# Performance work log

Hardware: AMD Instinct MI355X
Metric: run time of the kernel (lower is better)

Reference implementation:

```python
import jax, jax.numpy as jnp
import numpy as np

B, N, DIM, H, D, S = 4, 16384, 256, 8, 64, 64
INNER = H * D


def setup_inputs() -> dict:
    key = jax.random.key(0)
    ks = jax.random.split(key, 10)
    f = lambda k, shp, s: jax.random.normal(k, shp, jnp.float32) * s
    return {
        "x": jax.random.normal(ks[0], (B, N, DIM), jnp.float32),
        "Wx": f(ks[1], (INNER, DIM), 0.02), "bx": jnp.zeros((INNER,), jnp.float32),
        "Wfx": f(ks[2], (INNER, DIM), 0.02), "bfx": jnp.zeros((INNER,), jnp.float32),
        "Wslice": f(ks[3], (S, D), 0.125), "bslice": jnp.zeros((S,), jnp.float32),
        "temperature": jnp.full((1, H, 1, 1), 0.5, jnp.float32),
        "Wq": f(ks[4], (D, D), 0.125),
        "Wk": f(ks[5], (D, D), 0.125),
        "Wv": f(ks[6], (D, D), 0.125),
        "attn_scale": jnp.full((1, H, 1, 1), 10.0, jnp.float32),
        "slice_res_scale": jnp.full((1,), 0.1, jnp.float32),
        "Wout": f(ks[7], (DIM, INNER), 0.02), "bout": jnp.zeros((DIM,), jnp.float32),
    }


def reference(x, Wx, bx, Wfx, bfx, Wslice, bslice, temperature,
              Wq, Wk, Wv, attn_scale, slice_res_scale, Wout, bout):
    b, n, _ = x.shape
    # project and split heads -> [b, h, n, d]
    fx = (x @ Wfx.T + bfx).reshape(b, n, H, D).transpose(0, 2, 1, 3)
    xm = (x @ Wx.T + bx).reshape(b, n, H, D).transpose(0, 2, 1, 3)
    temp = jnp.clip(temperature, 1e-4)
    slice_logits = (xm @ Wslice.T + bslice) / temp              # [b,h,n,S]
    w = jax.nn.softmax(slice_logits, axis=-1)                   # slice weights
    slice_norm = w.sum(axis=2)                                  # [b,h,S]
    tok = jnp.einsum('bhnc,bhng->bhgc', fx, w)                  # [b,h,S,d]
    tok = tok / (slice_norm + 1e-5)[:, :, :, None]
    # small cross-slice attention (cosine, shared kv across heads)
    q = tok @ Wq.T                                              # [b,h,S,d]
    kv = tok.mean(axis=1, keepdims=True)                        # [b,1,S,d]
    k = kv @ Wk.T
    v = kv @ Wv.T
    qn = q / jnp.maximum(jnp.linalg.norm(q, axis=-1, keepdims=True), 1e-12)
    kn = k / jnp.maximum(jnp.linalg.norm(k, axis=-1, keepdims=True), 1e-12)
    logits = jnp.einsum('bhgd,bzsd->bhgs', qn, kn) * attn_scale  # z==1 broadcast
    attn = jax.nn.softmax(logits, axis=-1)
    out_tok = jnp.einsum('bhgs,bzsd->bhgd', attn, v)
    out_tok = out_tok + slice_res_scale * tok
    # broadcast slice tokens back to points
    out_x = jnp.einsum('bhgc,bhng->bhnc', out_tok, w)           # [b,h,n,d]
    out_x = out_x.transpose(0, 2, 1, 3).reshape(b, n, H * D)
    return out_x @ Wout.T + bout
```

## Files before the change

### kernel.cpp

```cpp
#include <hip/hip_runtime.h>
#include <math.h>

#define BQ   4
#define NTOK 16384
#define DIMM 256
#define HH   8
#define DDIM 64
#define SSL  64
#define INNERD 512
#define BN_TOK (BQ*NTOK)

typedef __attribute__((ext_vector_type(8))) short short8;
typedef __attribute__((ext_vector_type(4))) float f32x4;

__device__ inline float bf2f(unsigned short u) {
    union { float f; unsigned int i; } v; v.i = ((unsigned int)u) << 16; return v.f;
}
__device__ inline unsigned short f2bf(float f) {
    union { float f; unsigned int i; } v; v.f = f;
    unsigned int r = v.i + 0x7FFFu + ((v.i >> 16) & 1u);
    return (unsigned short)(r >> 16);
}

__device__ __forceinline__ void gl_lds16(const void* g, void* l) {
    __builtin_amdgcn_global_load_lds(
        (const __attribute__((address_space(1))) unsigned int*)g,
        (__attribute__((address_space(3))) unsigned int*)l, 16, 0, 0);
}

__global__ void k_prep(const float* __restrict__ Wx, const float* __restrict__ bx,
                       const float* __restrict__ Wfx, const float* __restrict__ bfx,
                       const float* __restrict__ Wslice, const float* __restrict__ bslice,
                       unsigned short* __restrict__ Wcatb, float* __restrict__ bcat)
{
    int row = blockIdx.x;
    int t = threadIdx.x;
    if (row < 512) {
        for (int c = t; c < 256; c += 64) Wcatb[row*256 + c] = f2bf(Wfx[row*256 + c]);
        if (t == 0) bcat[row] = bfx[row];
    } else {
        int r = row - 512, h = r >> 6, s = r & 63;
        for (int c = t; c < 256; c += 64) {
            float acc = 0.f;
            for (int d = 0; d < 64; ++d)
                acc += Wslice[s*64 + d] * Wx[(h*64 + d)*256 + c];
            Wcatb[row*256 + c] = f2bf(acc);
        }
        if (t == 0) {
            float acc = bslice[s];
            for (int d = 0; d < 64; ++d) acc += Wslice[s*64 + d] * bx[h*64 + d];
            bcat[row] = acc;
        }
    }
}

__global__ void k_xcast(const float* __restrict__ x, unsigned short* __restrict__ xb)
{
    size_t i = ((size_t)blockIdx.x*256 + threadIdx.x)*8;
    float4 a = *(const float4*)(x + i);
    float4 b = *(const float4*)(x + i + 4);
    *(ushort4*)(xb + i)     = make_ushort4(f2bf(a.x), f2bf(a.y), f2bf(a.z), f2bf(a.w));
    *(ushort4*)(xb + i + 4) = make_ushort4(f2bf(b.x), f2bf(b.y), f2bf(b.z), f2bf(b.w));
}

__global__ __launch_bounds__(256) void k_gemm1(
    const unsigned short* __restrict__ Xb, const unsigned short* __restrict__ Wb,
    const float* __restrict__ bias, const float* __restrict__ temperature,
    unsigned short* __restrict__ fx_t, unsigned short* __restrict__ wbuf)
{
    __shared__ unsigned short As[128*32];
    __shared__ unsigned short Bs[128*32];
    int bid = blockIdx.x;
    int rt = bid >> 3, ct = bid & 7;
    int m0 = rt*128, n0 = ct*128;
    int tid = threadIdx.x;
    int lane = tid & 63, w = tid >> 6;
    int wr = w >> 1, wc = w & 1;
    int lr = lane & 15, lq = lane >> 4;

    f32x4 acc[4][4];
#pragma unroll
    for (int i = 0; i < 4; i++)
#pragma unroll
        for (int j = 0; j < 4; j++) acc[i][j] = (f32x4)(0.f);

    int r0 = tid >> 2, kq0 = (tid & 3) * 8;

    for (int k0 = 0; k0 < 256; k0 += 32) {
        __syncthreads();
        gl_lds16(Xb + (size_t)(m0 + r0)*256 + k0 + kq0,      &As[(size_t)tid*8]);
        gl_lds16(Xb + (size_t)(m0 + 64 + r0)*256 + k0 + kq0, &As[(size_t)(tid+256)*8]);
        gl_lds16(Wb + (size_t)(n0 + r0)*256 + k0 + kq0,      &Bs[(size_t)tid*8]);
        gl_lds16(Wb + (size_t)(n0 + 64 + r0)*256 + k0 + kq0, &Bs[(size_t)(tid+256)*8]);
        __syncthreads();
        short8 af[4], bf[4];
#pragma unroll
        for (int i = 0; i < 4; i++) {
            af[i] = *(const short8*)&As[(wr*64 + i*16 + lr)*32 + lq*8];
            bf[i] = *(const short8*)&Bs[(wc*64 + i*16 + lr)*32 + lq*8];
        }
#pragma unroll
        for (int i = 0; i < 4; i++)
#pragma unroll
            for (int j = 0; j < 4; j++)
                acc[i][j] = __builtin_amdgcn_mfma_f32_16x16x32_bf16(af[i], bf[j], acc[i][j], 0, 0, 0);
    }

    float bv[4];
#pragma unroll
    for (int j = 0; j < 4; j++) bv[j] = bias[n0 + wc*64 + j*16 + lr];

    if (n0 < 512) {
        int h = (n0 + wc*64) >> 6;
        int batch = m0 >> 14;
#pragma unroll
        for (int i = 0; i < 4; i++) {
            int tokbase = m0 + wr*64 + i*16 + lq*4;
            int nloc = tokbase & (NTOK-1);
#pragma unroll
            for (int j = 0; j < 4; j++) {
                int d = j*16 + lr;
                ushort4 pk = make_ushort4(
                    f2bf(acc[i][j][0] + bv[j]), f2bf(acc[i][j][1] + bv[j]),
                    f2bf(acc[i][j][2] + bv[j]), f2bf(acc[i][j][3] + bv[j]));
                *(ushort4*)(fx_t + ((size_t)(batch*8 + h)*64 + d)*NTOK + nloc) = pk;
            }
        }
    } else {
        int h = (n0 - 512 + wc*64) >> 6;
        float it = 1.f / fmaxf(temperature[h], 1e-4f);
        int colbase = (n0 - 512) + wc*64;
#pragma unroll
        for (int i = 0; i < 4; i++) {
            int tokbase = m0 + wr*64 + i*16 + lq*4;
#pragma unroll
            for (int r = 0; r < 4; r++) {
                float v[4];
#pragma unroll
                for (int j = 0; j < 4; j++) v[j] = (acc[i][j][r] + bv[j]) * it;
                float mx = fmaxf(fmaxf(v[0], v[1]), fmaxf(v[2], v[3]));
                mx = fmaxf(mx, __shfl_xor(mx, 1));
                mx = fmaxf(mx, __shfl_xor(mx, 2));
                mx = fmaxf(mx, __shfl_xor(mx, 4));
                mx = fmaxf(mx, __shfl_xor(mx, 8));
                float e[4], sm = 0.f;
#pragma unroll
                for (int j = 0; j < 4; j++) { e[j] = __expf(v[j] - mx); sm += e[j]; }
                sm += __shfl_xor(sm, 1);
                sm += __shfl_xor(sm, 2);
                sm += __shfl_xor(sm, 4);
                sm += __shfl_xor(sm, 8);
                float inv = 1.f / sm;
                size_t rowoff = (size_t)(tokbase + r)*512 + colbase + lr;
#pragma unroll
                for (int j = 0; j < 4; j++)
                    wbuf[rowoff + j*16] = f2bf(e[j] * inv);
            }
        }
    }
}

__global__ __launch_bounds__(256) void k_tok(
    const unsigned short* __restrict__ wbuf, const unsigned short* __restrict__ fx_t,
    float* __restrict__ tok_acc, float* __restrict__ norm_acc)
{
    __shared__ unsigned short As[64*32];
    __shared__ unsigned short Bs[64*32];
    __shared__ float nsm[256];
    int chunk = blockIdx.x;
    int bh = blockIdx.y;
    int b = bh >> 3, h = bh & 7;
    int n0 = chunk * 512;
    int tid = threadIdx.x;
    int lane = tid & 63, w = tid >> 6;
    int lr = lane & 15, lq = lane >> 4;

    f32x4 acc[4];
#pragma unroll
    for (int j = 0; j < 4; j++) acc[j] = (f32x4)(0.f);
    float nacc = 0.f;

    int sN = tid & 63, qN = tid >> 6;

    for (int kk = 0; kk < 512; kk += 32) {
        __syncthreads();
        gl_lds16(fx_t + ((size_t)bh*64 + (tid>>2))*NTOK + n0 + kk + (tid&3)*8,
                 &Bs[(size_t)tid*8]);
        {
            int tk = tid >> 3;
            int s8 = (tid & 7) * 8;
            short8 g = *(const short8*)(wbuf +
                ((size_t)(b*NTOK + n0 + kk + tk))*512 + h*64 + s8);
#pragma unroll
            for (int j = 0; j < 8; j++)
                As[(s8 + j)*32 + tk] = ((unsigned short*)&g)[j];
        }
        __syncthreads();
        {
            float ns = 0.f;
#pragma unroll
            for (int k = 0; k < 8; k++) ns += bf2f(As[sN*32 + qN*8 + k]);
            nacc += ns;
        }
        short8 af = *(const short8*)&As[(w*16 + lr)*32 + lq*8];
#pragma unroll
        for (int j = 0; j < 4; j++) {
            short8 bf = *(const short8*)&Bs[(j*16 + lr)*32 + lq*8];
            acc[j] = __builtin_amdgcn_mfma_f32_16x16x32_bf16(af, bf, acc[j], 0, 0, 0);
        }
    }

#pragma unroll
    for (int j = 0; j < 4; j++) {
        int d = j*16 + lr;
#pragma unroll
        for (int r = 0; r < 4; r++) {
            int s = w*16 + lq*4 + r;
            atomicAdd(&tok_acc[((size_t)bh*64 + s)*64 + d], acc[j][r]);
        }
    }
    __syncthreads();
    nsm[tid] = nacc;
    __syncthreads();
    if (tid < 64)
        atomicAdd(&norm_acc[bh*64 + tid],
                  nsm[tid] + nsm[tid+64] + nsm[tid+128] + nsm[tid+192]);
}

__global__ void k_fintok(float* __restrict__ tok, const float* __restrict__ norm)
{
    int bh = blockIdx.x, tid = threadIdx.x;
    for (int idx = tid; idx < 4096; idx += 256) {
        int s = idx >> 6;
        tok[(size_t)bh*4096 + idx] /= (norm[bh*64 + s] + 1e-5f);
    }
}

__global__ __launch_bounds__(256) void k_kv(
    const float* __restrict__ tok, const float* __restrict__ Wk, const float* __restrict__ Wv,
    float* __restrict__ kn_out, float* __restrict__ v_out)
{
    __shared__ float KV[64][65];
    __shared__ float TMP[64][65];
    __shared__ float rn[64];
    int b = blockIdx.x, tid = threadIdx.x;
    for (int idx = tid; idx < 4096; idx += 256) {
        float s = 0.f;
        for (int h = 0; h < 8; ++h) s += tok[((size_t)(b*8 + h))*4096 + idx];
        KV[idx >> 6][idx & 63] = s * 0.125f;
    }
    __syncthreads();
    for (int idx = tid; idx < 4096; idx += 256) {
        int s = idx >> 6, d = idx & 63;
        float a = 0.f;
        for (int e = 0; e < 64; ++e) a += KV[s][e] * Wk[d*64 + e];
        TMP[s][d] = a;
    }
    __syncthreads();
    if (tid < 64) {
        float a = 0.f;
        for (int d = 0; d < 64; ++d) { float x = TMP[tid][d]; a += x*x; }
        rn[tid] = fmaxf(sqrtf(a), 1e-12f);
    }
    __syncthreads();
    for (int idx = tid; idx < 4096; idx += 256) {
        int s = idx >> 6, d = idx & 63;
        kn_out[(size_t)b*4096 + idx] = TMP[s][d] / rn[s];
    }
    for (int idx = tid; idx < 4096; idx += 256) {
        int s = idx >> 6, d = idx & 63;
        float a = 0.f;
        for (int e = 0; e < 64; ++e) a += KV[s][e] * Wv[d*64 + e];
        v_out[(size_t)b*4096 + idx] = a;
    }
}

__global__ __launch_bounds__(256) void k_attn(
    const float* __restrict__ tok, const float* __restrict__ Wq,
    const float* __restrict__ kn, const float* __restrict__ vbuf,
    const float* __restrict__ attn_scale, const float* __restrict__ srs,
    float* __restrict__ out_tok)
{
    __shared__ float Q[64][65];
    __shared__ float KN[64][65];
    __shared__ float L[64][65];
    __shared__ float rn[64];
    int h = blockIdx.x & 7, b = blockIdx.x >> 3;
    int bh = b*8 + h;
    int tid = threadIdx.x;
    for (int idx = tid; idx < 4096; idx += 256)
        KN[idx >> 6][idx & 63] = kn[(size_t)b*4096 + idx];
    __syncthreads();
    for (int idx = tid; idx < 4096; idx += 256) {
        int g = idx >> 6, d = idx & 63;
        float a = 0.f;
        for (int e = 0; e < 64; ++e) a += tok[(size_t)bh*4096 + g*64 + e] * Wq[d*64 + e];
        Q[g][d] = a;
    }
    __syncthreads();
    if (tid < 64) {
        float a = 0.f;
        for (int d = 0; d < 64; ++d) { float x = Q[tid][d]; a += x*x; }
        rn[tid] = fmaxf(sqrtf(a), 1e-12f);
    }
    __syncthreads();
    float scale = attn_scale[h];
    for (int idx = tid; idx < 4096; idx += 256) {
        int g = idx >> 6, s = idx & 63;
        float a = 0.f;
        for (int e = 0; e < 64; ++e) a += Q[g][e] * KN[s][e];
        L[g][s] = a / rn[g] * scale;
    }
    __syncthreads();
    if (tid < 64) {
        float mx = -1e30f;
        for (int s = 0; s < 64; ++s) mx = fmaxf(mx, L[tid][s]);
        float sm = 0.f;
        for (int s = 0; s < 64; ++s) { float e = expf(L[tid][s]-mx); L[tid][s] = e; sm += e; }
        float inv = 1.f/sm;
        for (int s = 0; s < 64; ++s) L[tid][s] *= inv;
    }
    __syncthreads();
    float srsv = srs[0];
    for (int idx = tid; idx < 4096; idx += 256) {
        int g = idx >> 6, d = idx & 63;
        float a = 0.f;
        for (int s = 0; s < 64; ++s) a += L[g][s] * vbuf[(size_t)b*4096 + s*64 + d];
        out_tok[(size_t)bh*4096 + idx] = a + srsv * tok[(size_t)bh*4096 + idx];
    }
}

__global__ __launch_bounds__(256) void k_mt(
    const float* __restrict__ out_tok, const float* __restrict__ Wout,
    unsigned short* __restrict__ MTb)
{
    __shared__ float Wt[64][68];
    __shared__ float Ot[64][68];
    int jt = blockIdx.x, h = blockIdx.y, b = blockIdx.z;
    int j0 = jt * 64;
    int tid = threadIdx.x;
    int tx = tid & 15, ty = tid >> 4;
#pragma unroll
    for (int i = 0; i < 4; i++) {
        int flat = tid + i*256;
        int r = flat >> 4;
        int c4 = (flat & 15) * 4;
        float4 wv = *(const float4*)(Wout + (size_t)(j0+r)*512 + h*64 + c4);
        Wt[c4+0][r]=wv.x; Wt[c4+1][r]=wv.y; Wt[c4+2][r]=wv.z; Wt[c4+3][r]=wv.w;
        float4 ov = *(const float4*)(out_tok + ((size_t)(b*8+h)*64 + r)*64 + c4);
        Ot[c4+0][r]=ov.x; Ot[c4+1][r]=ov.y; Ot[c4+2][r]=ov.z; Ot[c4+3][r]=ov.w;
    }
    __syncthreads();
    float acc[4][4] = {{0.f}};
#pragma unroll 8
    for (int d = 0; d < 64; ++d) {
        float av[4], bv[4];
        *(float4*)av = *(const float4*)&Wt[d][ty*4];
        *(float4*)bv = *(const float4*)&Ot[d][tx*4];
#pragma unroll
        for (int i = 0; i < 4; i++)
#pragma unroll
            for (int j = 0; j < 4; j++) acc[i][j] += av[i]*bv[j];
    }
#pragma unroll
    for (int i = 0; i < 4; i++) {
        int j = j0 + ty*4 + i;
#pragma unroll
        for (int jj = 0; jj < 4; jj++) {
            int s = tx*4 + jj;
            MTb[((size_t)(b*256) + j)*512 + h*64 + s] = f2bf(acc[i][jj]);
        }
    }
}

__global__ __launch_bounds__(256) void k_gemm2(
    const unsigned short* __restrict__ A, const unsigned short* __restrict__ Ball,
    const float* __restrict__ bias, float* __restrict__ C)
{
    __shared__ unsigned short As[128*32];
    __shared__ unsigned short Bs[128*32];
    int bid = blockIdx.x;
    int rt = bid >> 1, ct = bid & 1;
    int m0 = rt*128, n0 = ct*128;
    const unsigned short* Bm = Ball + (size_t)(m0 >> 14) * 256 * 512;
    int tid = threadIdx.x;
    int lane = tid & 63, w = tid >> 6;
    int wr = w >> 1, wc = w & 1;
    int lr = lane & 15, lq = lane >> 4;

    f32x4 acc[4][4];
#pragma unroll
    for (int i = 0; i < 4; i++)
#pragma unroll
        for (int j = 0; j < 4; j++) acc[i][j] = (f32x4)(0.f);

    int r0 = tid >> 2, kq0 = (tid & 3) * 8;

    for (int k0 = 0; k0 < 512; k0 += 32) {
        __syncthreads();
        gl_lds16(A + (size_t)(m0 + r0)*512 + k0 + kq0,       &As[(size_t)tid*8]);
        gl_lds16(A + (size_t)(m0 + 64 + r0)*512 + k0 + kq0,  &As[(size_t)(tid+256)*8]);
        gl_lds16(Bm + (size_t)(n0 + r0)*512 + k0 + kq0,      &Bs[(size_t)tid*8]);
        gl_lds16(Bm + (size_t)(n0 + 64 + r0)*512 + k0 + kq0, &Bs[(size_t)(tid+256)*8]);
        __syncthreads();
        short8 af[4], bf[4];
#pragma unroll
        for (int i = 0; i < 4; i++) {
            af[i] = *(const short8*)&As[(wr*64 + i*16 + lr)*32 + lq*8];
            bf[i] = *(const short8*)&Bs[(wc*64 + i*16 + lr)*32 + lq*8];
        }
#pragma unroll
        for (int i = 0; i < 4; i++)
#pragma unroll
            for (int j = 0; j < 4; j++)
                acc[i][j] = __builtin_amdgcn_mfma_f32_16x16x32_bf16(af[i], bf[j], acc[i][j], 0, 0, 0);
    }

#pragma unroll
    for (int j = 0; j < 4; j++) {
        int n = n0 + wc*64 + j*16 + lr;
        float bv = bias[n];
#pragma unroll
        for (int i = 0; i < 4; i++) {
            int mrow = m0 + wr*64 + i*16 + lq*4;
#pragma unroll
            for (int r = 0; r < 4; r++)
                C[(size_t)(mrow + r)*256 + n] = acc[i][j][r] + bv;
        }
    }
}

extern "C" void kernel_launch(void* const* d_in, const int* in_sizes, int n_in,
                              void* d_out, int out_size, void* d_ws, size_t ws_size,
                              hipStream_t stream)
{
    const float* x      = (const float*)d_in[0];
    const float* Wx     = (const float*)d_in[1];
    const float* bx     = (const float*)d_in[2];
    const float* Wfx    = (const float*)d_in[3];
    const float* bfx    = (const float*)d_in[4];
    const float* Wslice = (const float*)d_in[5];
    const float* bslice = (const float*)d_in[6];
    const float* temperature = (const float*)d_in[7];
    const float* Wq     = (const float*)d_in[8];
    const float* Wk     = (const float*)d_in[9];
    const float* Wv     = (const float*)d_in[10];
    const float* attn_scale = (const float*)d_in[11];
    const float* srs    = (const float*)d_in[12];
    const float* Wout   = (const float*)d_in[13];
    const float* bout   = (const float*)d_in[14];
    float* out = (float*)d_out;
    float* ws  = (float*)d_ws;

    float* tok  = ws + 0;
    float* norm = ws + 131072;
    float* bcat = ws + 133120;
    float* kn   = ws + 134144;
    float* vb   = ws + 150528;
    float* ot   = ws + 166912;
    unsigned short* Wcatb = (unsigned short*)(ws + 297984);
    unsigned short* MTb   = (unsigned short*)(ws + 429056);
    unsigned short* xb    = (unsigned short*)(ws + 691200);
    unsigned short* wbuf  = (unsigned short*)(ws + 9079808);
    unsigned short* fx_t  = (unsigned short*)d_out;

    hipMemsetAsync(tok, 0, 133120 * sizeof(float), stream);
    k_prep<<<1024, 64, 0, stream>>>(Wx, bx, Wfx, bfx, Wslice, bslice, Wcatb, bcat);
    k_xcast<<<8192, 256, 0, stream>>>(x, xb);
    k_gemm1<<<4096, 256, 0, stream>>>(xb, Wcatb, bcat, temperature, fx_t, wbuf);
    k_tok<<<dim3(32, 32), 256, 0, stream>>>(wbuf, fx_t, tok, norm);
    k_fintok<<<32, 256, 0, stream>>>(tok, norm);
    k_kv<<<4, 256, 0, stream>>>(tok, Wk, Wv, kn, vb);
    k_attn<<<32, 256, 0, stream>>>(tok, Wq, kn, vb, attn_scale, srs, ot);
    k_mt<<<dim3(4, 8, 4), 256, 0, stream>>>(ot, Wout, MTb);
    k_gemm2<<<1024, 256, 0, stream>>>(wbuf, MTb, bout, out);
}
```

Baseline: 419.7 us.

## Reassociate slice-token contraction to skip the fx projection, accumulate norms in gemm1

Drops the per-token fx projection. The slice tokens are now computed as (w^T x) @ Wfx^T plus norm-weighted bias, through a new k_tokY GEMM over a transposed bf16 copy of x and a small k_tokfin kernel. This halves the gemm1 output width. Slice-weight column sums move into the gemm1 epilogue via atomics, and gemm1 and gemm2 get an XCD-aware block remap. In exchange, k_tokY has a K=256 output per head with heavy atomic reductions, and the transposed x copy costs extra write bandwidth.

```diff
diff --git a/kernel.cpp b/kernel.cpp
--- a/kernel.cpp
+++ b/kernel.cpp
@@ -29,49 +29,75 @@
 }
 
 __global__ void k_prep(const float* __restrict__ Wx, const float* __restrict__ bx,
-                       const float* __restrict__ Wfx, const float* __restrict__ bfx,
                        const float* __restrict__ Wslice, const float* __restrict__ bslice,
-                       unsigned short* __restrict__ Wcatb, float* __restrict__ bcat)
+                       unsigned short* __restrict__ Wlogb, float* __restrict__ blog)
 {
     int row = blockIdx.x;
     int t = threadIdx.x;
-    if (row < 512) {
-        for (int c = t; c < 256; c += 64) Wcatb[row*256 + c] = f2bf(Wfx[row*256 + c]);
-        if (t == 0) bcat[row] = bfx[row];
-    } else {
-        int r = row - 512, h = r >> 6, s = r & 63;
-        for (int c = t; c < 256; c += 64) {
-            float acc = 0.f;
-            for (int d = 0; d < 64; ++d)
-                acc += Wslice[s*64 + d] * Wx[(h*64 + d)*256 + c];
-            Wcatb[row*256 + c] = f2bf(acc);
-        }
-        if (t == 0) {
-            float acc = bslice[s];
-            for (int d = 0; d < 64; ++d) acc += Wslice[s*64 + d] * bx[h*64 + d];
-            bcat[row] = acc;
-        }
-    }
-}
-
-__global__ void k_xcast(const float* __restrict__ x, unsigned short* __restrict__ xb)
-{
-    size_t i = ((size_t)blockIdx.x*256 + threadIdx.x)*8;
-    float4 a = *(const float4*)(x + i);
-    float4 b = *(const float4*)(x + i + 4);
-    *(ushort4*)(xb + i)     = make_ushort4(f2bf(a.x), f2bf(a.y), f2bf(a.z), f2bf(a.w));
-    *(ushort4*)(xb + i + 4) = make_ushort4(f2bf(b.x), f2bf(b.y), f2bf(b.z), f2bf(b.w));
+    int h = row >> 6, s = row & 63;
+    for (int c = t; c < 256; c += 64) {
+        float acc = 0.f;
+        for (int d = 0; d < 64; ++d)
+            acc += Wslice[s*64 + d] * Wx[(h*64 + d)*256 + c];
+        Wlogb[row*256 + c] = f2bf(acc);
+    }
+    if (t == 0) {
+        float acc = bslice[s];
+        for (int d = 0; d < 64; ++d) acc += Wslice[s*64 + d] * bx[h*64 + d];
+        blog[row] = acc;
+    }
+}
+
+__global__ __launch_bounds__(256) void k_xcast2(
+    const float* __restrict__ x, unsigned short* __restrict__ xb,
+    unsigned short* __restrict__ xbT)
+{
+    __shared__ unsigned short Xs[64*260];
+    int tb = blockIdx.x;
+    int tid = threadIdx.x;
+    const float* src = x + (size_t)tb*64*256;
+#pragma unroll
+    for (int i = 0; i < 16; i++) {
+        int f4 = i*256 + tid;
+        int tok = f4 >> 6, c4 = (f4 & 63)*4;
+        float4 v = *(const float4*)(src + (size_t)f4*4);
+        Xs[tok*260 + c4+0] = f2bf(v.x);
+        Xs[tok*260 + c4+1] = f2bf(v.y);
+        Xs[tok*260 + c4+2] = f2bf(v.z);
+        Xs[tok*260 + c4+3] = f2bf(v.w);
+    }
+    __syncthreads();
+    unsigned short* dxb = xb + (size_t)tb*64*256;
+#pragma unroll
+    for (int i = 0; i < 16; i++) {
+        int u4 = i*256 + tid;
+        int tok = u4 >> 6, c4 = (u4 & 63)*4;
+        *(ushort4*)(dxb + tok*256 + c4) = *(const ushort4*)&Xs[tok*260 + c4];
+    }
+    int b = (tb*64) >> 14;
+    int n0 = (tb*64) & (NTOK-1);
+    unsigned short* dxT = xbT + ((size_t)(b*256 + tid))*NTOK + n0;
+#pragma unroll
+    for (int i = 0; i < 16; i++) {
+        int t4 = i*4;
+        ushort4 v = make_ushort4(Xs[(t4+0)*260 + tid], Xs[(t4+1)*260 + tid],
+                                 Xs[(t4+2)*260 + tid], Xs[(t4+3)*260 + tid]);
+        *(ushort4*)(dxT + t4) = v;
+    }
 }
 
 __global__ __launch_bounds__(256) void k_gemm1(
     const unsigned short* __restrict__ Xb, const unsigned short* __restrict__ Wb,
     const float* __restrict__ bias, const float* __restrict__ temperature,
-    unsigned short* __restrict__ fx_t, unsigned short* __restrict__ wbuf)
+    unsigned short* __restrict__ wbuf, float* __restrict__ norm_acc)
 {
     __shared__ unsigned short As[128*32];
     __shared__ unsigned short Bs[128*32];
     int bid = blockIdx.x;
-    int rt = bid >> 3, ct = bid & 7;
+    int xcd = bid & 7;
+    int inner = bid >> 3;
+    int rt = xcd*64 + (inner >> 2);
+    int ct = inner & 3;
     int m0 = rt*128, n0 = ct*128;
     int tid = threadIdx.x;
     int lane = tid & 63, w = tid >> 6;
@@ -106,133 +132,133 @@
                 acc[i][j] = __builtin_amdgcn_mfma_f32_16x16x32_bf16(af[i], bf[j], acc[i][j], 0, 0, 0);
     }
 
+    int h = (n0 + wc*64) >> 6;
+    int batch = m0 >> 14;
+    float it = 1.f / fmaxf(temperature[h], 1e-4f);
     float bv[4];
 #pragma unroll
     for (int j = 0; j < 4; j++) bv[j] = bias[n0 + wc*64 + j*16 + lr];
-
-    if (n0 < 512) {
-        int h = (n0 + wc*64) >> 6;
-        int batch = m0 >> 14;
-#pragma unroll
-        for (int i = 0; i < 4; i++) {
-            int tokbase = m0 + wr*64 + i*16 + lq*4;
-            int nloc = tokbase & (NTOK-1);
+    float pn[4] = {0.f, 0.f, 0.f, 0.f};
+
+#pragma unroll
+    for (int i = 0; i < 4; i++) {
+        int tokbase = m0 + wr*64 + i*16 + lq*4;
+#pragma unroll
+        for (int r = 0; r < 4; r++) {
+            float v[4];
+#pragma unroll
+            for (int j = 0; j < 4; j++) v[j] = (acc[i][j][r] + bv[j]) * it;
+            float mx = fmaxf(fmaxf(v[0], v[1]), fmaxf(v[2], v[3]));
+            mx = fmaxf(mx, __shfl_xor(mx, 1));
+            mx = fmaxf(mx, __shfl_xor(mx, 2));
+            mx = fmaxf(mx, __shfl_xor(mx, 4));
+            mx = fmaxf(mx, __shfl_xor(mx, 8));
+            float e[4], sm = 0.f;
+#pragma unroll
+            for (int j = 0; j < 4; j++) { e[j] = __expf(v[j] - mx); sm += e[j]; }
+            sm += __shfl_xor(sm, 1);
+            sm += __shfl_xor(sm, 2);
+            sm += __shfl_xor(sm, 4);
+            sm += __shfl_xor(sm, 8);
+            float inv = 1.f / sm;
+            size_t rowoff = (size_t)(tokbase + r)*512 + n0 + wc*64 + lr;
 #pragma unroll
             for (int j = 0; j < 4; j++) {
-                int d = j*16 + lr;
-                ushort4 pk = make_ushort4(
-                    f2bf(acc[i][j][0] + bv[j]), f2bf(acc[i][j][1] + bv[j]),
-                    f2bf(acc[i][j][2] + bv[j]), f2bf(acc[i][j][3] + bv[j]));
-                *(ushort4*)(fx_t + ((size_t)(batch*8 + h)*64 + d)*NTOK + nloc) = pk;
+                float wv = e[j] * inv;
+                pn[j] += wv;
+                wbuf[rowoff + j*16] = f2bf(wv);
             }
         }
-    } else {
-        int h = (n0 - 512 + wc*64) >> 6;
-        float it = 1.f / fmaxf(temperature[h], 1e-4f);
-        int colbase = (n0 - 512) + wc*64;
-#pragma unroll
-        for (int i = 0; i < 4; i++) {
-            int tokbase = m0 + wr*64 + i*16 + lq*4;
-#pragma unroll
-            for (int r = 0; r < 4; r++) {
-                float v[4];
-#pragma unroll
-                for (int j = 0; j < 4; j++) v[j] = (acc[i][j][r] + bv[j]) * it;
-                float mx = fmaxf(fmaxf(v[0], v[1]), fmaxf(v[2], v[3]));
-                mx = fmaxf(mx, __shfl_xor(mx, 1));
-                mx = fmaxf(mx, __shfl_xor(mx, 2));
-                mx = fmaxf(mx, __shfl_xor(mx, 4));
-                mx = fmaxf(mx, __shfl_xor(mx, 8));
-                float e[4], sm = 0.f;
-#pragma unroll
-                for (int j = 0; j < 4; j++) { e[j] = __expf(v[j] - mx); sm += e[j]; }
-                sm += __shfl_xor(sm, 1);
-                sm += __shfl_xor(sm, 2);
-                sm += __shfl_xor(sm, 4);
-                sm += __shfl_xor(sm, 8);
-                float inv = 1.f / sm;
-                size_t rowoff = (size_t)(tokbase + r)*512 + colbase + lr;
-#pragma unroll
-                for (int j = 0; j < 4; j++)
-                    wbuf[rowoff + j*16] = f2bf(e[j] * inv);
-            }
-        }
-    }
-}
-
-__global__ __launch_bounds__(256) void k_tok(
-    const unsigned short* __restrict__ wbuf, const unsigned short* __restrict__ fx_t,
-    float* __restrict__ tok_acc, float* __restrict__ norm_acc)
+    }
+#pragma unroll
+    for (int j = 0; j < 4; j++) {
+        pn[j] += __shfl_xor(pn[j], 16);
+        pn[j] += __shfl_xor(pn[j], 32);
+    }
+    if (lane < 16) {
+#pragma unroll
+        for (int j = 0; j < 4; j++)
+            atomicAdd(&norm_acc[(batch*8 + h)*64 + j*16 + lr], pn[j]);
+    }
+}
+
+__global__ __launch_bounds__(256) void k_tokY(
+    const unsigned short* __restrict__ wbuf, const unsigned short* __restrict__ xbT,
+    float* __restrict__ Y)
 {
     __shared__ unsigned short As[64*32];
-    __shared__ unsigned short Bs[64*32];
-    __shared__ float nsm[256];
+    __shared__ unsigned short Bs[256*32];
     int chunk = blockIdx.x;
     int bh = blockIdx.y;
     int b = bh >> 3, h = bh & 7;
-    int n0 = chunk * 512;
     int tid = threadIdx.x;
     int lane = tid & 63, w = tid >> 6;
     int lr = lane & 15, lq = lane >> 4;
 
-    f32x4 acc[4];
-#pragma unroll
-    for (int j = 0; j < 4; j++) acc[j] = (f32x4)(0.f);
-    float nacc = 0.f;
-
-    int sN = tid & 63, qN = tid >> 6;
-
-    for (int kk = 0; kk < 512; kk += 32) {
+    f32x4 acc[4][4];
+#pragma unroll
+    for (int i = 0; i < 4; i++)
+#pragma unroll
+        for (int j = 0; j < 4; j++) acc[i][j] = (f32x4)(0.f);
+
+    int tk = tid >> 3, s8 = (tid & 7)*8;
+    int crow = tid >> 2, nn = (tid & 3)*8;
+    size_t wrowbase = ((size_t)(b*NTOK + chunk*2048))*512 + h*64 + s8;
+    const unsigned short* xTb = xbT + (size_t)b*256*NTOK + chunk*2048;
+
+    for (int kk = 0; kk < 2048; kk += 32) {
         __syncthreads();
-        gl_lds16(fx_t + ((size_t)bh*64 + (tid>>2))*NTOK + n0 + kk + (tid&3)*8,
-                 &Bs[(size_t)tid*8]);
-        {
-            int tk = tid >> 3;
-            int s8 = (tid & 7) * 8;
-            short8 g = *(const short8*)(wbuf +
-                ((size_t)(b*NTOK + n0 + kk + tk))*512 + h*64 + s8);
-#pragma unroll
-            for (int j = 0; j < 8; j++)
-                As[(s8 + j)*32 + tk] = ((unsigned short*)&g)[j];
+#pragma unroll
+        for (int q = 0; q < 4; q++)
+            gl_lds16(xTb + (size_t)(q*64 + crow)*NTOK + kk + nn,
+                     &Bs[q*2048 + (size_t)tid*8]);
+        short8 g = *(const short8*)(wbuf + wrowbase + (size_t)(kk + tk)*512);
+#pragma unroll
+        for (int j = 0; j < 8; j++)
+            As[(s8 + j)*32 + tk] = ((unsigned short*)&g)[j];
+        __syncthreads();
+        short8 af[4], bfr[4];
+#pragma unroll
+        for (int i = 0; i < 4; i++)
+            af[i] = *(const short8*)&As[(i*16 + lr)*32 + lq*8];
+#pragma unroll
+        for (int j = 0; j < 4; j++)
+            bfr[j] = *(const short8*)&Bs[(w*64 + j*16 + lr)*32 + lq*8];
+#pragma unroll
+        for (int i = 0; i < 4; i++)
+#pragma unroll
+            for (int j = 0; j < 4; j++)
+                acc[i][j] = __builtin_amdgcn_mfma_f32_16x16x32_bf16(af[i], bfr[j], acc[i][j], 0, 0, 0);
+    }
+
+#pragma unroll
+    for (int i = 0; i < 4; i++)
+#pragma unroll
+        for (int j = 0; j < 4; j++) {
+            int c = w*64 + j*16 + lr;
+#pragma unroll
+            for (int r = 0; r < 4; r++) {
+                int s = i*16 + lq*4 + r;
+                atomicAdd(&Y[((size_t)bh*64 + s)*256 + c], acc[i][j][r]);
+            }
         }
-        __syncthreads();
-        {
-            float ns = 0.f;
-#pragma unroll
-            for (int k = 0; k < 8; k++) ns += bf2f(As[sN*32 + qN*8 + k]);
-            nacc += ns;
-        }
-        short8 af = *(const short8*)&As[(w*16 + lr)*32 + lq*8];
-#pragma unroll
-        for (int j = 0; j < 4; j++) {
-            short8 bf = *(const short8*)&Bs[(j*16 + lr)*32 + lq*8];
-            acc[j] = __builtin_amdgcn_mfma_f32_16x16x32_bf16(af, bf, acc[j], 0, 0, 0);
-        }
-    }
-
-#pragma unroll
-    for (int j = 0; j < 4; j++) {
-        int d = j*16 + lr;
-#pragma unroll
-        for (int r = 0; r < 4; r++) {
-            int s = w*16 + lq*4 + r;
-            atomicAdd(&tok_acc[((size_t)bh*64 + s)*64 + d], acc[j][r]);
-        }
-    }
-    __syncthreads();
-    nsm[tid] = nacc;
-    __syncthreads();
-    if (tid < 64)
-        atomicAdd(&norm_acc[bh*64 + tid],
-                  nsm[tid] + nsm[tid+64] + nsm[tid+128] + nsm[tid+192]);
-}
-
-__global__ void k_fintok(float* __restrict__ tok, const float* __restrict__ norm)
-{
-    int bh = blockIdx.x, tid = threadIdx.x;
-    for (int idx = tid; idx < 4096; idx += 256) {
-        int s = idx >> 6;
-        tok[(size_t)bh*4096 + idx] /= (norm[bh*64 + s] + 1e-5f);
+}
+
+__global__ __launch_bounds__(256) void k_tokfin(
+    const float* __restrict__ Y, const float* __restrict__ norm_,
+    const float* __restrict__ Wfx, const float* __restrict__ bfx,
+    float* __restrict__ tok)
+{
+    int bh = blockIdx.x; int h = bh & 7;
+    int tid = threadIdx.x;
+    for (int idx = tid; idx < 4096; idx += 256) {
+        int d = idx >> 6, s = idx & 63;
+        const float* yr = Y + ((size_t)bh*64 + s)*256;
+        const float* wr = Wfx + (size_t)(h*64 + d)*256;
+        float a = 0.f;
+        for (int c = 0; c < 256; ++c) a += yr[c] * wr[c];
+        float nv = norm_[bh*64 + s];
+        tok[(size_t)bh*4096 + s*64 + d] = (a + nv*bfx[h*64 + d]) / (nv + 1e-5f);
     }
 }
 
@@ -317,8 +343,8 @@
         for (int s = 0; s < 64; ++s) mx = fmaxf(mx, L[tid][s]);
         float sm = 0.f;
         for (int s = 0; s < 64; ++s) { float e = expf(L[tid][s]-mx); L[tid][s] = e; sm += e; }
-        float inv = 1.f/sm;
-        for (int s = 0; s < 64; ++s) L[tid][s] *= inv;
+        float ivv = 1.f/sm;
+        for (int s = 0; s < 64; ++s) L[tid][s] *= ivv;
     }
     __syncthreads();
     float srsv = srs[0];
@@ -380,7 +406,10 @@
     __shared__ unsigned short As[128*32];
     __shared__ unsigned short Bs[128*32];
     int bid = blockIdx.x;
-    int rt = bid >> 1, ct = bid & 1;
+    int xcd = bid & 7;
+    int inner = bid >> 3;
+    int rt = xcd*64 + (inner >> 1);
+    int ct = inner & 1;
     int m0 = rt*128, n0 = ct*128;
     const unsigned short* Bm = Ball + (size_t)(m0 >> 14) * 256 * 512;
     int tid = threadIdx.x;
@@ -452,26 +481,29 @@
     float* out = (float*)d_out;
     float* ws  = (float*)d_ws;
 
-    float* tok  = ws + 0;
-    float* norm = ws + 131072;
-    float* bcat = ws + 133120;
-    float* kn   = ws + 134144;
-    float* vb   = ws + 150528;
-    float* ot   = ws + 166912;
-    unsigned short* Wcatb = (unsigned short*)(ws + 297984);
-    unsigned short* MTb   = (unsigned short*)(ws + 429056);
-    unsigned short* xb    = (unsigned short*)(ws + 691200);
-    unsigned short* wbuf  = (unsigned short*)(ws + 9079808);
-    unsigned short* fx_t  = (unsigned short*)d_out;
-
-    hipMemsetAsync(tok, 0, 133120 * sizeof(float), stream);
-    k_prep<<<1024, 64, 0, stream>>>(Wx, bx, Wfx, bfx, Wslice, bslice, Wcatb, bcat);
-    k_xcast<<<8192, 256, 0, stream>>>(x, xb);
-    k_gemm1<<<4096, 256, 0, stream>>>(xb, Wcatb, bcat, temperature, fx_t, wbuf);
-    k_tok<<<dim3(32, 32), 256, 0, stream>>>(wbuf, fx_t, tok, norm);
-    k_fintok<<<32, 256, 0, stream>>>(tok, norm);
-    k_kv<<<4, 256, 0, stream>>>(tok, Wk, Wv, kn, vb);
-    k_attn<<<32, 256, 0, stream>>>(tok, Wq, kn, vb, attn_scale, srs, ot);
-    k_mt<<<dim3(4, 8, 4), 256, 0, stream>>>(ot, Wout, MTb);
-    k_gemm2<<<1024, 256, 0, stream>>>(wbuf, MTb, bout, out);
-}
+    float* Y    = ws + 0;
+    float* norm = ws + 524288;
+    float* blog = ws + 526336;
+    float* kn   = ws + 527360;
+    float* vb   = ws + 543744;
+    float* ot   = ws + 560128;
+    float* tok  = ws + 691200;
+    unsigned short* Wlogb = (unsigned short*)(ws + 822272);
+    unsigned short* MTb   = (unsigned short*)(ws + 887808);
+    unsigned short* xb    = (unsigned short*)(ws + 1149952);
+    unsigned short* xbT   = (unsigned short*)(ws + 9538560);
+
+    hipMemsetAsync(Y, 0, (524288 + 2048) * sizeof(float), stream);
+    k_prep<<<512, 64, 0, stream>>>(Wx, bx, Wslice, bslice, Wlogb, blog);
+    k_xcast2<<<1024, 256, 0, stream>>>(x, xb, xbT);
+    k_gemm1<<<2048, 256, 0, stream>>>(xb, Wlogb, blog, temperature, (unsigned short*)(ws + 9538560 + 8388608), norm);
+    {
+        unsigned short* wbuf = (unsigned short*)(ws + 9538560 + 8388608);
+        k_tokY<<<dim3(8, 32), 256, 0, stream>>>(wbuf, xbT, Y);
+        k_tokfin<<<32, 256, 0, stream>>>(Y, norm, Wfx, bfx, tok);
+        k_kv<<<4, 256, 0, stream>>>(tok, Wk, Wv, kn, vb);
+        k_attn<<<32, 256, 0, stream>>>(tok, Wq, kn, vb, attn_scale, srs, ot);
+        k_mt<<<dim3(4, 8, 4), 256, 0, stream>>>(ot, Wout, MTb);
+        k_gemm2<<<1024, 256, 0, stream>>>(wbuf, MTb, bout, out);
+    }
+}
```

Measured after the change: 578.6 us. 1.38x slower.
